# Optimization experiments

Hardware: AMD Instinct MI355X
Metric: run time of the kernel (lower is better)

The kernel has to match this reference:

```python
import jax, jax.numpy as jnp
import numpy as np

# shift search range (matches init_kwargs)
MIN_SX, MAX_SX = -4, 4
MIN_SY, MAX_SY = -4, 4
B, C, H, W = 4, 3, 512, 512


def _shift(x, sx, sy):
    """torch.roll on dims (1,2) of a [C,H,W] tensor, zeroing wrapped rows/cols.

    Equivalent to AutomatedShiftFix.shift: positive sx zeros rows [:sx],
    negative sx zeros rows [sx:]; same for sy on the W axis.
    """
    h, w = x.shape[1], x.shape[2]
    shifted = jnp.roll(x, (sx, sy), axis=(1, 2))
    i = jnp.arange(h)[:, None]   # [H,1]
    j = jnp.arange(w)[None, :]   # [1,W]
    mask_h = jnp.where(sx >= 0, i >= sx, i < h + sx)
    mask_w = jnp.where(sy >= 0, j >= sy, j < w + sy)
    mask = (mask_h & mask_w).astype(x.dtype)  # [H,W]
    return shifted * mask[None]


def _all_shifts():
    sx = jnp.arange(MIN_SX, MAX_SX + 1)
    sy = jnp.arange(MIN_SY, MAX_SY + 1)
    # outer loop over shift_x, inner over shift_y -> 'ij' matches torch ordering
    return jnp.stack(jnp.meshgrid(sx, sy, indexing="ij"), axis=-1).reshape(-1, 2)  # [Ns,2]


def setup_inputs() -> dict:
    key = jax.random.key(0)
    k1, k2 = jax.random.split(key)
    x_ref = jax.random.normal(k1, (B, C, H, W), dtype=jnp.float32)
    x = jax.random.normal(k2, (B, C, H, W), dtype=jnp.float32)
    return {"x_ref": x_ref, "x": x}


def reference(x_ref, x):
    shifts = _all_shifts()  # [Ns,2] int32

    def sims_one(xr, xi):  # xr, xi: [C,H,W]
        # similarity for every candidate shift: sum over (C,H,W) of shifted*ref
        return jax.vmap(lambda s: jnp.sum(_shift(xi, s[0], s[1]) * xr))(shifts)  # [Ns]

    sims = jax.vmap(sims_one)(x_ref, x)          # [B, Ns]
    best = jnp.argmax(sims, axis=1)              # [B]
    best_shifts = shifts[best]                   # [B, 2]
    out = jax.vmap(lambda xi, s: _shift(xi, s[0], s[1]))(x, best_shifts)  # [B,C,H,W]
    return out, best_shifts
```

## Files before the change

### kernel.cpp

```cpp
#include <hip/hip_runtime.h>

#define BB 4
#define CC 3
#define HH 512
#define WW 512
#define NS 81
#define IMG (HH * WW)
#define CHW (CC * IMG)
#define STRIP 16
#define NSTRIPS (HH / STRIP)
#define NBLK (BB * CC * NSTRIPS)
#define SLOTS (CC * NSTRIPS)

__device__ double g_part[(size_t)BB * NS * SLOTS];
__device__ int    g_best[BB];

#define C4(v, i) ((i) == 0 ? (v).x : (i) == 1 ? (v).y : (i) == 2 ? (v).z : (v).w)

__global__ __launch_bounds__(576) void k_sims(const float* __restrict__ xref,
                                              const float* __restrict__ x) {
    int bid   = blockIdx.x;
    int strip = bid % NSTRIPS;
    int bc    = bid / NSTRIPS;
    int b     = bc / CC;
    const float* xp = x    + (size_t)bc * IMG;
    const float* rp = xref + (size_t)bc * IMG;
    int tid  = threadIdx.x;
    int lane = tid & 63;
    int sxi  = tid >> 6;
    int j0   = lane << 3;
    int sx   = sxi - 4;
    int ip0  = strip * STRIP;

    float acc[9];
#pragma unroll
    for (int s = 0; s < 9; ++s) acc[s] = 0.f;

#pragma unroll
    for (int rr = 0; rr < STRIP; ++rr) {
        int ip = ip0 + rr;
        int ii = ip + sx;
        if ((unsigned)ii >= HH) continue;

        const float* xrow = xp + ip * WW + j0;
        const float* rrow = rp + ii * WW + j0;
        float4 xa = *(const float4*)(xrow);
        float4 xb = *(const float4*)(xrow + 4);
        float4 ra = *(const float4*)(rrow);
        float4 rb = *(const float4*)(rrow + 4);

        float p0 = __shfl_up(rb.x, 1, 64);
        float p1 = __shfl_up(rb.y, 1, 64);
        float p2 = __shfl_up(rb.z, 1, 64);
        float p3 = __shfl_up(rb.w, 1, 64);
        if (lane == 0) { p0 = p1 = p2 = p3 = 0.f; }
        float n0 = __shfl_down(ra.x, 1, 64);
        float n1 = __shfl_down(ra.y, 1, 64);
        float n2 = __shfl_down(ra.z, 1, 64);
        float n3 = __shfl_down(ra.w, 1, 64);
        if (lane == 63) { n0 = n1 = n2 = n3 = 0.f; }

#define P4(i) ((i) == 0 ? p0 : (i) == 1 ? p1 : (i) == 2 ? p2 : p3)
#define N4(i) ((i) == 0 ? n0 : (i) == 1 ? n1 : (i) == 2 ? n2 : n3)
#pragma unroll
        for (int syi = 0; syi < 9; ++syi) {
#pragma unroll
            for (int k = 0; k < 8; ++k) {
                int i = k + syi;
                float wv = (i < 4)  ? P4(i)
                         : (i < 8)  ? C4(ra, i - 4)
                         : (i < 12) ? C4(rb, i - 8)
                         :            N4(i - 12);
                float xv = (k < 4) ? C4(xa, k) : C4(xb, k - 4);
                acc[syi] += xv * wv;
            }
        }
#undef P4
#undef N4
    }

    int cs = (bc % CC) * NSTRIPS + strip;
#pragma unroll
    for (int s = 0; s < 9; ++s) {
        float v = acc[s];
        for (int off = 32; off; off >>= 1) v += __shfl_down(v, off, 64);
        if (lane == 0)
            g_part[((size_t)b * NS + sxi * 9 + s) * SLOTS + cs] = (double)v;
    }
}

__global__ __launch_bounds__(128) void k_reduce(float* __restrict__ outTail) {
    int b = blockIdx.x;
    int t = threadIdx.x;
    __shared__ double vals[NS];
    if (t < NS) {
        const double* p = g_part + ((size_t)b * NS + t) * SLOTS;
        double s = 0.0;
        for (int i = 0; i < SLOTS; ++i) s += p[i];
        vals[t] = s;
    }
    __syncthreads();
    if (t == 0) {
        int best = 0;
        double bv = vals[0];
        for (int i = 1; i < NS; ++i)
            if (vals[i] > bv) { bv = vals[i]; best = i; }
        g_best[b] = best;
        outTail[b * 2]     = (float)(best / 9 - 4);
        outTail[b * 2 + 1] = (float)(best % 9 - 4);
    }
}

__global__ __launch_bounds__(256) void k_apply(const float* __restrict__ x,
                                               float* __restrict__ out) {
    int blk = blockIdx.x;
    int bc  = blk >> 8;
    int tid = threadIdx.x;
    int b   = bc / CC;

    int bi = g_best[b];
    int sx = bi / 9 - 4;
    int sy = bi % 9 - 4;

    int row = ((blk & 255) << 1) + (tid >> 7);
    int j0  = (tid & 127) << 2;
    int is  = row - sx;
    float4 v = make_float4(0.f, 0.f, 0.f, 0.f);
    if ((unsigned)is < HH) {
        const float* src = x + (size_t)bc * IMG + is * WW;
        int js0 = j0 - sy;
        if (js0 >= 0 && js0 + 3 < WW) {
            v = *(const float4*)(src + js0);
        } else {
            float* vv = (float*)&v;
#pragma unroll
            for (int k = 0; k < 4; ++k) {
                int js = js0 + k;
                if ((unsigned)js < WW) vv[k] = src[js];
            }
        }
    }
    *(float4*)(out + (size_t)bc * IMG + row * WW + j0) = v;
}

extern "C" void kernel_launch(void* const* d_in, const int* in_sizes, int n_in,
                              void* d_out, int out_size, void* d_ws, size_t ws_size,
                              hipStream_t stream) {
    const float* xref = (const float*)d_in[0];
    const float* x    = (const float*)d_in[1];
    float* out = (float*)d_out;
    (void)d_ws; (void)ws_size;

    k_sims<<<NBLK, 576, 0, stream>>>(xref, x);
    k_reduce<<<BB, 128, 0, stream>>>(out + (size_t)BB * CHW);

    int applyBlocks = (BB * CC * HH) / 2;
    k_apply<<<applyBlocks, 256, 0, stream>>>(x, out);
}
```

Measured before the change: 96.51 us.

## Fold channels into sims blocks with software-prefetched rows and single-block reduce

```diff
diff --git a/kernel.cpp b/kernel.cpp
--- a/kernel.cpp
+++ b/kernel.cpp
@@ -7,24 +7,21 @@
 #define NS 81
 #define IMG (HH * WW)
 #define CHW (CC * IMG)
-#define STRIP 16
+#define STRIP 8
 #define NSTRIPS (HH / STRIP)
-#define NBLK (BB * CC * NSTRIPS)
-#define SLOTS (CC * NSTRIPS)
+#define NBLK (BB * NSTRIPS)
+#define NROWS (CC * STRIP)
 
-__device__ double g_part[(size_t)BB * NS * SLOTS];
+__device__ double g_part[NSTRIPS][BB * NS];
 __device__ int    g_best[BB];
 
 #define C4(v, i) ((i) == 0 ? (v).x : (i) == 1 ? (v).y : (i) == 2 ? (v).z : (v).w)
 
-__global__ __launch_bounds__(576) void k_sims(const float* __restrict__ xref,
-                                              const float* __restrict__ x) {
+__global__ __launch_bounds__(576, 8) void k_sims(const float* __restrict__ xref,
+                                                 const float* __restrict__ x) {
     int bid   = blockIdx.x;
-    int strip = bid % NSTRIPS;
-    int bc    = bid / NSTRIPS;
-    int b     = bc / CC;
-    const float* xp = x    + (size_t)bc * IMG;
-    const float* rp = xref + (size_t)bc * IMG;
+    int strip = bid & (NSTRIPS - 1);
+    int b     = bid >> 6;
     int tid  = threadIdx.x;
     int lane = tid & 63;
     int sxi  = tid >> 6;
@@ -32,82 +29,101 @@
     int sx   = sxi - 4;
     int ip0  = strip * STRIP;
 
+    const float* xbase = x    + (size_t)b * CHW;
+    const float* rbase = xref + (size_t)b * CHW;
+
     float acc[9];
 #pragma unroll
     for (int s = 0; s < 9; ++s) acc[s] = 0.f;
 
-#pragma unroll
-    for (int rr = 0; rr < STRIP; ++rr) {
-        int ip = ip0 + rr;
-        int ii = ip + sx;
-        if ((unsigned)ii >= HH) continue;
+    float4 xa, xb, ra, rb, nxa, nxb, nra, nrb;
+    bool okc;
+    {
+        int ii = ip0 + sx;
+        okc = (unsigned)ii < HH;
+        const float* xr = xbase + ip0 * WW + j0;
+        const float* rr_ = rbase + (okc ? ii : ip0) * WW + j0;
+        xa = *(const float4*)xr;   xb = *(const float4*)(xr + 4);
+        ra = *(const float4*)rr_;  rb = *(const float4*)(rr_ + 4);
+    }
 
-        const float* xrow = xp + ip * WW + j0;
-        const float* rrow = rp + ii * WW + j0;
-        float4 xa = *(const float4*)(xrow);
-        float4 xb = *(const float4*)(xrow + 4);
-        float4 ra = *(const float4*)(rrow);
-        float4 rb = *(const float4*)(rrow + 4);
+#pragma unroll 2
+    for (int t = 0; t < NROWS; ++t) {
+        bool okn = false;
+        if (t < NROWS - 1) {
+            int tn = t + 1;
+            int c  = tn >> 3;
+            int ip = ip0 + (tn & 7);
+            int ii = ip + sx;
+            okn = (unsigned)ii < HH;
+            const float* xr  = xbase + (size_t)c * IMG + ip * WW + j0;
+            const float* rr_ = rbase + (size_t)c * IMG + (okn ? ii : ip) * WW + j0;
+            nxa = *(const float4*)xr;   nxb = *(const float4*)(xr + 4);
+            nra = *(const float4*)rr_;  nrb = *(const float4*)(rr_ + 4);
+        }
 
-        float p0 = __shfl_up(rb.x, 1, 64);
-        float p1 = __shfl_up(rb.y, 1, 64);
-        float p2 = __shfl_up(rb.z, 1, 64);
-        float p3 = __shfl_up(rb.w, 1, 64);
-        if (lane == 0) { p0 = p1 = p2 = p3 = 0.f; }
-        float n0 = __shfl_down(ra.x, 1, 64);
-        float n1 = __shfl_down(ra.y, 1, 64);
-        float n2 = __shfl_down(ra.z, 1, 64);
-        float n3 = __shfl_down(ra.w, 1, 64);
-        if (lane == 63) { n0 = n1 = n2 = n3 = 0.f; }
+        if (okc) {
+            float p0 = __shfl_up(rb.x, 1, 64);
+            float p1 = __shfl_up(rb.y, 1, 64);
+            float p2 = __shfl_up(rb.z, 1, 64);
+            float p3 = __shfl_up(rb.w, 1, 64);
+            if (lane == 0) { p0 = p1 = p2 = p3 = 0.f; }
+            float n0 = __shfl_down(ra.x, 1, 64);
+            float n1 = __shfl_down(ra.y, 1, 64);
+            float n2 = __shfl_down(ra.z, 1, 64);
+            float n3 = __shfl_down(ra.w, 1, 64);
+            if (lane == 63) { n0 = n1 = n2 = n3 = 0.f; }
 
 #define P4(i) ((i) == 0 ? p0 : (i) == 1 ? p1 : (i) == 2 ? p2 : p3)
 #define N4(i) ((i) == 0 ? n0 : (i) == 1 ? n1 : (i) == 2 ? n2 : n3)
 #pragma unroll
-        for (int syi = 0; syi < 9; ++syi) {
+            for (int syi = 0; syi < 9; ++syi) {
 #pragma unroll
-            for (int k = 0; k < 8; ++k) {
-                int i = k + syi;
-                float wv = (i < 4)  ? P4(i)
-                         : (i < 8)  ? C4(ra, i - 4)
-                         : (i < 12) ? C4(rb, i - 8)
-                         :            N4(i - 12);
-                float xv = (k < 4) ? C4(xa, k) : C4(xb, k - 4);
-                acc[syi] += xv * wv;
+                for (int k = 0; k < 8; ++k) {
+                    int i = k + syi;
+                    float wv = (i < 4)  ? P4(i)
+                             : (i < 8)  ? C4(ra, i - 4)
+                             : (i < 12) ? C4(rb, i - 8)
+                             :            N4(i - 12);
+                    float xv = (k < 4) ? C4(xa, k) : C4(xb, k - 4);
+                    acc[syi] += xv * wv;
+                }
             }
-        }
 #undef P4
 #undef N4
+        }
+
+        xa = nxa; xb = nxb; ra = nra; rb = nrb; okc = okn;
     }
 
-    int cs = (bc % CC) * NSTRIPS + strip;
 #pragma unroll
     for (int s = 0; s < 9; ++s) {
         float v = acc[s];
         for (int off = 32; off; off >>= 1) v += __shfl_down(v, off, 64);
         if (lane == 0)
-            g_part[((size_t)b * NS + sxi * 9 + s) * SLOTS + cs] = (double)v;
+            g_part[strip][b * NS + sxi * 9 + s] = (double)v;
     }
 }
 
-__global__ __launch_bounds__(128) void k_reduce(float* __restrict__ outTail) {
-    int b = blockIdx.x;
+__global__ __launch_bounds__(384) void k_reduce(float* __restrict__ outTail) {
     int t = threadIdx.x;
-    __shared__ double vals[NS];
-    if (t < NS) {
-        const double* p = g_part + ((size_t)b * NS + t) * SLOTS;
+    __shared__ double vals[BB * NS];
+    if (t < BB * NS) {
         double s = 0.0;
-        for (int i = 0; i < SLOTS; ++i) s += p[i];
+#pragma unroll 4
+        for (int k = 0; k < NSTRIPS; ++k) s += g_part[k][t];
         vals[t] = s;
     }
     __syncthreads();
-    if (t == 0) {
+    if (t < BB) {
+        const double* v = vals + t * NS;
         int best = 0;
-        double bv = vals[0];
+        double bv = v[0];
         for (int i = 1; i < NS; ++i)
-            if (vals[i] > bv) { bv = vals[i]; best = i; }
-        g_best[b] = best;
-        outTail[b * 2]     = (float)(best / 9 - 4);
-        outTail[b * 2 + 1] = (float)(best % 9 - 4);
+            if (v[i] > bv) { bv = v[i]; best = i; }
+        g_best[t] = best;
+        outTail[t * 2]     = (float)(best / 9 - 4);
+        outTail[t * 2 + 1] = (float)(best % 9 - 4);
     }
 }
 
@@ -152,7 +168,7 @@
     (void)d_ws; (void)ws_size;
 
     k_sims<<<NBLK, 576, 0, stream>>>(xref, x);
-    k_reduce<<<BB, 128, 0, stream>>>(out + (size_t)BB * CHW);
+    k_reduce<<<1, 384, 0, stream>>>(out + (size_t)BB * CHW);
 
     int applyBlocks = (BB * CC * HH) / 2;
     k_apply<<<applyBlocks, 256, 0, stream>>>(x, out);
```

Measured after the change: 96.54 us. Within noise of the previous version (+0.0%).
